# Kernel tuning notes

Hardware: AMD Instinct MI355X
Metric: run time of the kernel (lower is better)

Reference implementation:

```python
import jax, jax.numpy as jnp
import numpy as np

B, S, HID = 2, 4096, 1024
NH, HD = 16, 64
R = 2  # dilation_rate


def setup_inputs() -> dict:
    key = jax.random.key(0)
    ks = jax.random.split(key, 6)
    sc = 0.02
    return {
        "hidden_states": jax.random.normal(ks[0], (B, S, HID), jnp.float32),
        "Wq": jax.random.normal(ks[1], (HID, HID), jnp.float32) * sc,
        "Wk": jax.random.normal(ks[2], (HID, HID), jnp.float32) * sc,
        "Wv": jax.random.normal(ks[3], (HID, HID), jnp.float32) * sc,
        "Wo": jax.random.normal(ks[4], (HID, HID), jnp.float32) * sc,
        "bo": jnp.zeros((HID,), jnp.float32),
    }


def reference(hidden_states, Wq, Wk, Wv, Wo, bo):
    bsz, q_len, _ = hidden_states.shape
    # projections (torch Linear: y = x @ W.T)
    q = jnp.einsum('bsh,oh->bso', hidden_states, Wq).reshape(bsz, q_len, NH, HD).transpose(0, 2, 1, 3)
    k = jnp.einsum('bsh,oh->bso', hidden_states, Wk).reshape(bsz, q_len, NH, HD).transpose(0, 2, 1, 3)
    v = jnp.einsum('bsh,oh->bso', hidden_states, Wv).reshape(bsz, q_len, NH, HD).transpose(0, 2, 1, 3)
    # strided dilation gather (indices 0, R, 2R, ...)
    q = q[:, :, ::R, :]
    k = k[:, :, ::R, :]
    v = v[:, :, ::R, :]
    sd = q.shape[2]  # dilated length
    # SDPA with is_causal=True over the dilated subsequence
    scores = jnp.einsum('bhqd,bhkd->bhqk', q, k) / np.sqrt(HD).astype(np.float32)
    causal = jnp.tril(jnp.ones((sd, sd), bool))
    scores = jnp.where(causal, scores, jnp.finfo(scores.dtype).min)
    probs = jax.nn.softmax(scores, axis=-1)
    attn = jnp.einsum('bhqk,bhkd->bhqd', probs, v)  # [B, H, sd, HD]
    attn = attn.transpose(0, 2, 1, 3).reshape(bsz, sd, HID)
    # scatter back into zero-initialized full-length tensor
    full = jnp.zeros((bsz, q_len, HID), attn.dtype).at[:, ::R, :].set(attn)
    return jnp.einsum('bsh,oh->bso', full, Wo) + bo
```

## Files before the change

### kernel.cpp

```cpp
#include <hip/hip_runtime.h>
#include <cstdint>

typedef unsigned short u16;
typedef unsigned int u32;
typedef __attribute__((ext_vector_type(8))) short short8;
typedef __attribute__((ext_vector_type(4))) float f32x4;
typedef __attribute__((ext_vector_type(4))) unsigned short u16x4;
typedef __attribute__((ext_vector_type(4))) u32 u32x4;
typedef __attribute__((ext_vector_type(2))) u32 u32x2;

#define S_ 4096
#define SD 2048

__device__ __forceinline__ u16 f2bf(float f) {
  union { float f; u32 u; } v; v.f = f;
  u32 r = v.u + 0x7fffu + ((v.u >> 16) & 1u);
  return (u16)(r >> 16);
}
#if __has_builtin(__builtin_amdgcn_cvt_pk_bf16_f32)
__device__ __forceinline__ u32 pkbf(float a, float b) {
  auto r = __builtin_amdgcn_cvt_pk_bf16_f32(a, b);
  u32 o; __builtin_memcpy(&o, &r, 4); return o;
}
#else
__device__ __forceinline__ u32 pkbf(float a, float b) {
  union { float f; u32 u; } ua, ub; ua.f = a; ub.f = b;
  return __builtin_amdgcn_perm(ub.u + 0x8000u, ua.u + 0x8000u, 0x07060302u);
}
#endif
__device__ __forceinline__ f32x4 mfma16(short8 a, short8 b, f32x4 c) {
  return __builtin_amdgcn_mfma_f32_16x16x32_bf16(a, b, c, 0, 0, 0);
}
__device__ __forceinline__ void async16(const void* g, void* l) {
  __builtin_amdgcn_global_load_lds((__attribute__((address_space(1))) void*)g,
                                   (__attribute__((address_space(3))) void*)l,
                                   16, 0, 0);
}

__global__ __launch_bounds__(256) void cast_all(const float* __restrict__ hs,
                                                const float* __restrict__ Wq,
                                                const float* __restrict__ Wk,
                                                const float* __restrict__ Wv,
                                                const float* __restrict__ Wo,
                                                u16* __restrict__ dstW,
                                                u16* __restrict__ dstX) {
  int bid = blockIdx.x;
  if (bid < 4096) {
    int gid = bid * 256 + threadIdx.x;
    int wsel = gid >> 18;
    int off  = (gid & 262143) * 4;
    const float* src = (wsel == 0) ? Wq : (wsel == 1) ? Wk : (wsel == 2) ? Wv : Wo;
    float scl = (wsel == 0) ? 0.18033688f : 1.0f;
    f32x4 v = *(const f32x4*)(src + off);
    u16x4 o; o.x = f2bf(v.x * scl); o.y = f2bf(v.y * scl);
    o.z = f2bf(v.z * scl); o.w = f2bf(v.w * scl);
    *(u16x4*)(dstW + (size_t)wsel * 1048576 + off) = o;
  } else {
    int gid = (bid - 4096) * 256 + threadIdx.x;
    int e = gid * 4;
    int m = e >> 10, col = e & 1023;
    int b = m >> 11, sm = m & 2047;
    const float* src = hs + ((size_t)(b * S_ + 2 * sm) << 10) + col;
    f32x4 v = *(const f32x4*)src;
    u16x4 o; o.x = f2bf(v.x); o.y = f2bf(v.y); o.z = f2bf(v.z); o.w = f2bf(v.w);
    *(u16x4*)(dstX + ((size_t)m << 10) + col) = o;
  }
}

__device__ __forceinline__ void gemm_body128(const u16* __restrict__ A,
                                             const u16* __restrict__ B,
                                             u16* __restrict__ C, int N,
                                             int bm, int bn, char* lA, char* lB) {
  const int tid = threadIdx.x, lane = tid & 63, w = tid >> 6;
  const int quad = lane >> 4, l15 = lane & 15;
  const int wm = (w & 1) * 64, wn = (w >> 1) * 64;
  f32x4 acc[4][4] = {};

  auto stage = [&](int buf, int k0) {
#pragma unroll
    for (int i = 0; i < 2; i++) {
      int p = i * 256 + tid;
      int row = p >> 2, cp = p & 3;
      int c = cp ^ ((row ^ (row >> 2)) & 3);
      async16(A + (size_t)(bm + row) * 1024 + k0 + c * 8,
              lA + buf * 8192 + i * 4096 + w * 1024);
      async16(B + (size_t)(bn + row) * 1024 + k0 + c * 8,
              lB + buf * 8192 + i * 4096 + w * 1024);
    }
  };

  stage(0, 0);
#pragma unroll 1
  for (int kt = 0; kt < 32; kt++) {
    __syncthreads();
    if (kt + 1 < 32) stage((kt + 1) & 1, (kt + 1) * 32);
    const char* A_ = lA + (kt & 1) * 8192;
    const char* B_ = lB + (kt & 1) * 8192;
    short8 af[4], bf[4];
#pragma unroll
    for (int mi = 0; mi < 4; mi++) {
      int row = wm + mi * 16 + l15;
      af[mi] = *(const short8*)(A_ + (row * 4 + (quad ^ ((row ^ (row >> 2)) & 3))) * 16);
    }
#pragma unroll
    for (int ni = 0; ni < 4; ni++) {
      int row = wn + ni * 16 + l15;
      bf[ni] = *(const short8*)(B_ + (row * 4 + (quad ^ ((row ^ (row >> 2)) & 3))) * 16);
    }
#pragma unroll
    for (int mi = 0; mi < 4; mi++)
#pragma unroll
      for (int ni = 0; ni < 4; ni++)
        acc[mi][ni] = mfma16(af[mi], bf[ni], acc[mi][ni]);
  }
#pragma unroll
  for (int mi = 0; mi < 4; mi++)
#pragma unroll
    for (int ni = 0; ni < 4; ni++) {
      int m0 = bm + wm + mi * 16 + quad * 4;
      int n = bn + wn + ni * 16 + l15;
#pragma unroll
      for (int r = 0; r < 4; r++)
        C[(size_t)(m0 + r) * N + n] = f2bf(acc[mi][ni][r]);
    }
}

__global__ __launch_bounds__(256) void qkv_gemm(const u16* __restrict__ X,
                                                const u16* __restrict__ Wbf,
                                                u16* __restrict__ QK,
                                                u16* __restrict__ Vt) {
  __shared__ __align__(16) char lA[16384];
  __shared__ __align__(16) char lB[16384];
  int bid = blockIdx.x;
  if (bid < 512) {
    gemm_body128(X, Wbf, QK, 2048, (bid >> 4) * 128, (bid & 15) * 128, lA, lB);
  } else {
    int b2 = bid - 512;
    gemm_body128(Wbf + 2 * 1048576, X, Vt, 4096, (b2 >> 5) * 128, (b2 & 31) * 128, lA, lB);
  }
}

__global__ __launch_bounds__(256) void oproj(const u16* __restrict__ A,
                                             const u16* __restrict__ B,
                                             const float* __restrict__ bo,
                                             float* __restrict__ out) {
  __shared__ __align__(16) char lA[8192];
  __shared__ __align__(16) char lB[8192];
  const int tid = threadIdx.x, lane = tid & 63, w = tid >> 6;
  const int quad = lane >> 4, l15 = lane & 15;
  const int bm = blockIdx.y * 64, bn = blockIdx.x * 64;
  const int wm = (w & 1) * 32, wn = (w >> 1) * 32;
  f32x4 acc[2][2] = {};

  auto stage = [&](int buf, int k0) {
    int row = tid >> 2, cp = tid & 3;
    int c = cp ^ ((row ^ (row >> 2)) & 3);
    async16(A + (size_t)(bm + row) * 1024 + k0 + c * 8, lA + buf * 4096 + w * 1024);
    async16(B + (size_t)(bn + row) * 1024 + k0 + c * 8, lB + buf * 4096 + w * 1024);
  };

  stage(0, 0);
#pragma unroll 1
  for (int kt = 0; kt < 32; kt++) {
    __syncthreads();
    if (kt + 1 < 32) stage((kt + 1) & 1, (kt + 1) * 32);
    const char* A_ = lA + (kt & 1) * 4096;
    const char* B_ = lB + (kt & 1) * 4096;
    short8 af[2], bf[2];
#pragma unroll
    for (int mi = 0; mi < 2; mi++) {
      int row = wm + mi * 16 + l15;
      af[mi] = *(const short8*)(A_ + (row * 4 + (quad ^ ((row ^ (row >> 2)) & 3))) * 16);
    }
#pragma unroll
    for (int ni = 0; ni < 2; ni++) {
      int row = wn + ni * 16 + l15;
      bf[ni] = *(const short8*)(B_ + (row * 4 + (quad ^ ((row ^ (row >> 2)) & 3))) * 16);
    }
#pragma unroll
    for (int mi = 0; mi < 2; mi++)
#pragma unroll
      for (int ni = 0; ni < 2; ni++)
        acc[mi][ni] = mfma16(af[mi], bf[ni], acc[mi][ni]);
  }
#pragma unroll
  for (int mi = 0; mi < 2; mi++)
#pragma unroll
    for (int ni = 0; ni < 2; ni++) {
      int n = bn + wn + ni * 16 + l15;
      float bias = bo[n];
#pragma unroll
      for (int r = 0; r < 4; r++) {
        int m = bm + wm + mi * 16 + quad * 4 + r;
        int bb = m >> 11, sm = m & 2047;
        size_t grow = ((size_t)(bb * S_ + 2 * sm)) << 10;
        out[grow + n] = acc[mi][ni][r] + bias;
        out[grow + 1024 + n] = bias;
      }
    }
}

__global__ __launch_bounds__(256) void attn6(const u16* __restrict__ QK,
                                             const u16* __restrict__ Vt,
                                             u16* __restrict__ O) {
  __shared__ __align__(16) char lK[2][8192];
  __shared__ __align__(16) char lV[2][8192];
  const int tid = threadIdx.x, lane = tid & 63, w = tid >> 6;
  const int quad = lane >> 4, l15 = lane & 15;
  const int h = blockIdx.x, b = blockIdx.y;
  const int qt = 31 - (int)blockIdx.z;
  const int qb = qt * 64 + w * 16;

  const u16* qp = QK + (size_t)(b * SD + qb + l15) * 2048 + h * 64 + quad * 8;
  short8 qf0 = *(const short8*)qp;
  short8 qf1 = *(const short8*)(qp + 32);

  auto stageK = [&](int buf, int kb) {
#pragma unroll
    for (int i = 0; i < 2; i++) {
      int p = (w * 2 + i) * 64 + lane;
      int row = p >> 3, c = (p & 7) ^ (row & 7);
      async16(QK + (size_t)(b * SD + kb + row) * 2048 + 1024 + h * 64 + c * 8,
              lK[buf] + (w * 2 + i) * 1024);
    }
  };

  const int vd = tid >> 2, vg = tid & 3;
  const u16* vgbase = Vt + (size_t)(h * 64 + vd) * 4096 + b * SD;
  const int vs = vd & 7;
  const int cb0 = (vg & 1) * 2;
  const int cb1 = cb0 + 4;
  const int inn = (vg >> 1) * 8;
  const int aw0 = vd * 128 + ((cb0     ^ vs) * 16) + inn;
  const int aw1 = vd * 128 + (((cb0+1) ^ vs) * 16) + inn;
  const int aw2 = vd * 128 + ((cb1     ^ vs) * 16) + inn;
  const int aw3 = vd * 128 + (((cb1+1) ^ vs) * 16) + inn;

  u32x4 nv0, nv1;
  auto loadV = [&](int kb) {
    nv0 = *(const u32x4*)(vgbase + kb + vg * 8);
    nv1 = *(const u32x4*)(vgbase + kb + 32 + vg * 8);
  };
  auto writeV = [&](int buf) {
    char* Vn = lV[buf];
    *(u32x2*)(Vn + aw0) = u32x2{nv0.x, nv0.y};
    *(u32x2*)(Vn + aw1) = u32x2{nv0.z, nv0.w};
    *(u32x2*)(Vn + aw2) = u32x2{nv1.x, nv1.y};
    *(u32x2*)(Vn + aw3) = u32x2{nv1.z, nv1.w};
  };

  f32x4 oacc[4] = {};
  float l4[4] = {0.f, 0.f, 0.f, 0.f};

  stageK(0, 0);
  loadV(0);
  writeV(0);

#pragma unroll 1
  for (int kt = 0; kt <= qt; kt++) {
    __syncthreads();
    if (kt + 1 <= qt) {
      stageK((kt + 1) & 1, (kt + 1) * 64);
      loadV((kt + 1) * 64);
    }
    const char* K_ = lK[kt & 1];
    const char* V_ = lV[kt & 1];

    f32x4 s[4];
#pragma unroll
    for (int m = 0; m < 4; m++) {
      int key = m * 16 + l15;
      short8 kf0 = *(const short8*)(K_ + (key * 8 + (quad ^ (key & 7))) * 16);
      short8 kf1 = *(const short8*)(K_ + (key * 8 + ((4 + quad) ^ (key & 7))) * 16);
      f32x4 a = {};
      a = mfma16(kf0, qf0, a);
      a = mfma16(kf1, qf1, a);
      s[m] = a;
    }
    if (kt == qt) {
      int qrel = w * 16 + l15;
#pragma unroll
      for (int m = 0; m < 4; m++)
#pragma unroll
        for (int r = 0; r < 4; r++)
          if (m * 16 + quad * 4 + r > qrel) s[m][r] = -1e30f;
    }
    float pr[4][4];
#pragma unroll
    for (int m = 0; m < 4; m++) {
#pragma unroll
      for (int r = 0; r < 4; r++) pr[m][r] = exp2f(s[m][r]);
      l4[m] += (pr[m][0] + pr[m][1]) + (pr[m][2] + pr[m][3]);
    }
    u32 pw[8];
#pragma unroll
    for (int m = 0; m < 4; m++) {
      pw[m * 2]     = pkbf(pr[m][0], pr[m][1]);
      pw[m * 2 + 1] = pkbf(pr[m][2], pr[m][3]);
    }
    short8 pf0, pf1;
    __builtin_memcpy(&pf0, &pw[0], 16);
    __builtin_memcpy(&pf1, &pw[4], 16);

#pragma unroll
    for (int m = 0; m < 4; m++) {
      int dr = m * 16 + l15;
      short8 vf0 = *(const short8*)(V_ + (dr * 128 + ((quad     ^ (dr & 7)) * 16)));
      short8 vf1 = *(const short8*)(V_ + (dr * 128 + (((4+quad) ^ (dr & 7)) * 16)));
      oacc[m] = mfma16(vf0, pf0, oacc[m]);
      oacc[m] = mfma16(vf1, pf1, oacc[m]);
    }
    if (kt + 1 <= qt) writeV((kt + 1) & 1);
  }

  float l = (l4[0] + l4[1]) + (l4[2] + l4[3]);
  l += __shfl_xor(l, 16, 64);
  l += __shfl_xor(l, 32, 64);
  float inv = 1.0f / l;
  u16* op = O + (size_t)(b * SD + qb + l15) * 1024 + h * 64;
#pragma unroll
  for (int m = 0; m < 4; m++) {
    u16x4 ov;
#pragma unroll
    for (int r = 0; r < 4; r++) ov[r] = f2bf(oacc[m][r] * inv);
    *(u16x4*)(op + m * 16 + quad * 4) = ov;
  }
}

extern "C" void kernel_launch(void* const* d_in, const int* in_sizes, int n_in,
                              void* d_out, int out_size, void* d_ws, size_t ws_size,
                              hipStream_t stream) {
  (void)in_sizes; (void)n_in; (void)out_size; (void)ws_size;
  const float* hs = (const float*)d_in[0];
  const float* Wq = (const float*)d_in[1];
  const float* Wk = (const float*)d_in[2];
  const float* Wv = (const float*)d_in[3];
  const float* Wo = (const float*)d_in[4];
  const float* bo = (const float*)d_in[5];
  float* out = (float*)d_out;
  char* ws = (char*)d_ws;

  u16* Xbf = (u16*)ws;
  u16* Wbf = (u16*)(ws + (8u << 20));
  u16* QKb = (u16*)(ws + (16u << 20));
  u16* Vtb = (u16*)(ws + (32u << 20));
  u16* Ob  = (u16*)(ws + (40u << 20));

  cast_all<<<8192, 256, 0, stream>>>(hs, Wq, Wk, Wv, Wo, Wbf, Xbf);
  qkv_gemm<<<768, 256, 0, stream>>>(Xbf, Wbf, QKb, Vtb);
  attn6<<<dim3(16, 2, 32), 256, 0, stream>>>(QKb, Vtb, Ob);
  oproj<<<dim3(16, 64), 256, 0, stream>>>(Ob, Wbf + 3 * 1048576, bo, out);
}
```

Before: 190.6 us.

## Halve attention block to two waves each handling two query subtiles

The attention kernel now runs with 128 threads per block, and each wave computes two 16-row query subtiles. This lets every K and V fragment read from LDS feed twice as many MFMAs, cutting LDS traffic per FLOP. The V tile in LDS gains a padded row stride of 144 bytes to reduce bank conflicts, and exp2 now uses the hardware builtin when available. The trade-off is higher register pressure from doubled accumulators and fewer waves per block to hide latency.

```diff
diff --git a/kernel.cpp b/kernel.cpp
--- a/kernel.cpp
+++ b/kernel.cpp
@@ -27,6 +27,11 @@
   union { float f; u32 u; } ua, ub; ua.f = a; ub.f = b;
   return __builtin_amdgcn_perm(ub.u + 0x8000u, ua.u + 0x8000u, 0x07060302u);
 }
+#endif
+#if __has_builtin(__builtin_amdgcn_exp2f)
+__device__ __forceinline__ float fexp2(float x) { return __builtin_amdgcn_exp2f(x); }
+#else
+__device__ __forceinline__ float fexp2(float x) { return exp2f(x); }
 #endif
 __device__ __forceinline__ f32x4 mfma16(short8 a, short8 b, f32x4 c) {
   return __builtin_amdgcn_mfma_f32_16x16x32_bf16(a, b, c, 0, 0, 0);
@@ -200,57 +205,60 @@
     }
 }
 
-__global__ __launch_bounds__(256) void attn6(const u16* __restrict__ QK,
+#define VSTR 144
+__global__ __launch_bounds__(128) void attn7(const u16* __restrict__ QK,
                                              const u16* __restrict__ Vt,
                                              u16* __restrict__ O) {
   __shared__ __align__(16) char lK[2][8192];
-  __shared__ __align__(16) char lV[2][8192];
+  __shared__ __align__(16) char lV[2][64 * VSTR];
   const int tid = threadIdx.x, lane = tid & 63, w = tid >> 6;
   const int quad = lane >> 4, l15 = lane & 15;
   const int h = blockIdx.x, b = blockIdx.y;
   const int qt = 31 - (int)blockIdx.z;
-  const int qb = qt * 64 + w * 16;
-
-  const u16* qp = QK + (size_t)(b * SD + qb + l15) * 2048 + h * 64 + quad * 8;
-  short8 qf0 = *(const short8*)qp;
-  short8 qf1 = *(const short8*)(qp + 32);
+  const int qb = qt * 64;
+
+  short8 qf0[2], qf1[2];
+#pragma unroll
+  for (int s = 0; s < 2; s++) {
+    const u16* qp = QK + (size_t)(b * SD + qb + s * 32 + w * 16 + l15) * 2048 + h * 64 + quad * 8;
+    qf0[s] = *(const short8*)qp;
+    qf1[s] = *(const short8*)(qp + 32);
+  }
 
   auto stageK = [&](int buf, int kb) {
 #pragma unroll
-    for (int i = 0; i < 2; i++) {
-      int p = (w * 2 + i) * 64 + lane;
+    for (int i = 0; i < 4; i++) {
+      int p = i * 128 + tid;
       int row = p >> 3, c = (p & 7) ^ (row & 7);
       async16(QK + (size_t)(b * SD + kb + row) * 2048 + 1024 + h * 64 + c * 8,
-              lK[buf] + (w * 2 + i) * 1024);
-    }
-  };
-
-  const int vd = tid >> 2, vg = tid & 3;
+              lK[buf] + i * 2048 + w * 1024);
+    }
+  };
+
+  const int vd = tid >> 1, half = tid & 1;
+  const int vs = vd & 7;
   const u16* vgbase = Vt + (size_t)(h * 64 + vd) * 4096 + b * SD;
-  const int vs = vd & 7;
-  const int cb0 = (vg & 1) * 2;
-  const int cb1 = cb0 + 4;
-  const int inn = (vg >> 1) * 8;
-  const int aw0 = vd * 128 + ((cb0     ^ vs) * 16) + inn;
-  const int aw1 = vd * 128 + (((cb0+1) ^ vs) * 16) + inn;
-  const int aw2 = vd * 128 + ((cb1     ^ vs) * 16) + inn;
-  const int aw3 = vd * 128 + (((cb1+1) ^ vs) * 16) + inn;
-
-  u32x4 nv0, nv1;
+  u32x4 q0, q1, q2, q3;
   auto loadV = [&](int kb) {
-    nv0 = *(const u32x4*)(vgbase + kb + vg * 8);
-    nv1 = *(const u32x4*)(vgbase + kb + 32 + vg * 8);
+    q0 = *(const u32x4*)(vgbase + kb + half * 16);
+    q1 = *(const u32x4*)(vgbase + kb + half * 16 + 8);
+    q2 = *(const u32x4*)(vgbase + kb + 32 + half * 16);
+    q3 = *(const u32x4*)(vgbase + kb + 32 + half * 16 + 8);
   };
   auto writeV = [&](int buf) {
-    char* Vn = lV[buf];
-    *(u32x2*)(Vn + aw0) = u32x2{nv0.x, nv0.y};
-    *(u32x2*)(Vn + aw1) = u32x2{nv0.z, nv0.w};
-    *(u32x2*)(Vn + aw2) = u32x2{nv1.x, nv1.y};
-    *(u32x2*)(Vn + aw3) = u32x2{nv1.z, nv1.w};
-  };
-
-  f32x4 oacc[4] = {};
-  float l4[4] = {0.f, 0.f, 0.f, 0.f};
+    char* Vn = lV[buf] + vd * VSTR + half * 8;
+    *(u32x2*)(Vn + ((0 ^ vs) * 16)) = u32x2{q0.x, q0.y};
+    *(u32x2*)(Vn + ((1 ^ vs) * 16)) = u32x2{q0.z, q0.w};
+    *(u32x2*)(Vn + ((2 ^ vs) * 16)) = u32x2{q1.x, q1.y};
+    *(u32x2*)(Vn + ((3 ^ vs) * 16)) = u32x2{q1.z, q1.w};
+    *(u32x2*)(Vn + ((4 ^ vs) * 16)) = u32x2{q2.x, q2.y};
+    *(u32x2*)(Vn + ((5 ^ vs) * 16)) = u32x2{q2.z, q2.w};
+    *(u32x2*)(Vn + ((6 ^ vs) * 16)) = u32x2{q3.x, q3.y};
+    *(u32x2*)(Vn + ((7 ^ vs) * 16)) = u32x2{q3.z, q3.w};
+  };
+
+  f32x4 oacc[2][4] = {};
+  float l4[2][4] = {};
 
   stageK(0, 0);
   loadV(0);
@@ -266,64 +274,79 @@
     const char* K_ = lK[kt & 1];
     const char* V_ = lV[kt & 1];
 
-    f32x4 s[4];
+    f32x4 s[2][4];
 #pragma unroll
     for (int m = 0; m < 4; m++) {
       int key = m * 16 + l15;
       short8 kf0 = *(const short8*)(K_ + (key * 8 + (quad ^ (key & 7))) * 16);
       short8 kf1 = *(const short8*)(K_ + (key * 8 + ((4 + quad) ^ (key & 7))) * 16);
-      f32x4 a = {};
-      a = mfma16(kf0, qf0, a);
-      a = mfma16(kf1, qf1, a);
-      s[m] = a;
+#pragma unroll
+      for (int st = 0; st < 2; st++) {
+        f32x4 a = {};
+        a = mfma16(kf0, qf0[st], a);
+        a = mfma16(kf1, qf1[st], a);
+        s[st][m] = a;
+      }
     }
     if (kt == qt) {
-      int qrel = w * 16 + l15;
-#pragma unroll
-      for (int m = 0; m < 4; m++)
-#pragma unroll
-        for (int r = 0; r < 4; r++)
-          if (m * 16 + quad * 4 + r > qrel) s[m][r] = -1e30f;
-    }
-    float pr[4][4];
-#pragma unroll
-    for (int m = 0; m < 4; m++) {
-#pragma unroll
-      for (int r = 0; r < 4; r++) pr[m][r] = exp2f(s[m][r]);
-      l4[m] += (pr[m][0] + pr[m][1]) + (pr[m][2] + pr[m][3]);
-    }
-    u32 pw[8];
-#pragma unroll
-    for (int m = 0; m < 4; m++) {
-      pw[m * 2]     = pkbf(pr[m][0], pr[m][1]);
-      pw[m * 2 + 1] = pkbf(pr[m][2], pr[m][3]);
-    }
-    short8 pf0, pf1;
-    __builtin_memcpy(&pf0, &pw[0], 16);
-    __builtin_memcpy(&pf1, &pw[4], 16);
+#pragma unroll
+      for (int st = 0; st < 2; st++) {
+        int qrel = st * 32 + w * 16 + l15;
+#pragma unroll
+        for (int m = 0; m < 4; m++)
+#pragma unroll
+          for (int r = 0; r < 4; r++)
+            if (m * 16 + quad * 4 + r > qrel) s[st][m][r] = -1e30f;
+      }
+    }
+    short8 pf0[2], pf1[2];
+#pragma unroll
+    for (int st = 0; st < 2; st++) {
+      float pr[4][4];
+#pragma unroll
+      for (int m = 0; m < 4; m++) {
+#pragma unroll
+        for (int r = 0; r < 4; r++) pr[m][r] = fexp2(s[st][m][r]);
+        l4[st][m] += (pr[m][0] + pr[m][1]) + (pr[m][2] + pr[m][3]);
+      }
+      u32 pw[8];
+#pragma unroll
+      for (int m = 0; m < 4; m++) {
+        pw[m * 2]     = pkbf(pr[m][0], pr[m][1]);
+        pw[m * 2 + 1] = pkbf(pr[m][2], pr[m][3]);
+      }
+      __builtin_memcpy(&pf0[st], &pw[0], 16);
+      __builtin_memcpy(&pf1[st], &pw[4], 16);
+    }
 
 #pragma unroll
     for (int m = 0; m < 4; m++) {
       int dr = m * 16 + l15;
-      short8 vf0 = *(const short8*)(V_ + (dr * 128 + ((quad     ^ (dr & 7)) * 16)));
-      short8 vf1 = *(const short8*)(V_ + (dr * 128 + (((4+quad) ^ (dr & 7)) * 16)));
-      oacc[m] = mfma16(vf0, pf0, oacc[m]);
-      oacc[m] = mfma16(vf1, pf1, oacc[m]);
+      short8 vf0 = *(const short8*)(V_ + dr * VSTR + ((quad       ^ (dr & 7)) * 16));
+      short8 vf1 = *(const short8*)(V_ + dr * VSTR + (((4 + quad) ^ (dr & 7)) * 16));
+#pragma unroll
+      for (int st = 0; st < 2; st++) {
+        oacc[st][m] = mfma16(vf0, pf0[st], oacc[st][m]);
+        oacc[st][m] = mfma16(vf1, pf1[st], oacc[st][m]);
+      }
     }
     if (kt + 1 <= qt) writeV((kt + 1) & 1);
   }
 
-  float l = (l4[0] + l4[1]) + (l4[2] + l4[3]);
-  l += __shfl_xor(l, 16, 64);
-  l += __shfl_xor(l, 32, 64);
-  float inv = 1.0f / l;
-  u16* op = O + (size_t)(b * SD + qb + l15) * 1024 + h * 64;
-#pragma unroll
-  for (int m = 0; m < 4; m++) {
-    u16x4 ov;
-#pragma unroll
-    for (int r = 0; r < 4; r++) ov[r] = f2bf(oacc[m][r] * inv);
-    *(u16x4*)(op + m * 16 + quad * 4) = ov;
+#pragma unroll
+  for (int st = 0; st < 2; st++) {
+    float l = (l4[st][0] + l4[st][1]) + (l4[st][2] + l4[st][3]);
+    l += __shfl_xor(l, 16, 64);
+    l += __shfl_xor(l, 32, 64);
+    float inv = 1.0f / l;
+    u16* op = O + (size_t)(b * SD + qb + st * 32 + w * 16 + l15) * 1024 + h * 64;
+#pragma unroll
+    for (int m = 0; m < 4; m++) {
+      u16x4 ov;
+#pragma unroll
+      for (int r = 0; r < 4; r++) ov[r] = f2bf(oacc[st][m][r] * inv);
+      *(u16x4*)(op + m * 16 + quad * 4) = ov;
+    }
   }
 }
 
@@ -348,6 +371,6 @@
 
   cast_all<<<8192, 256, 0, stream>>>(hs, Wq, Wk, Wv, Wo, Wbf, Xbf);
   qkv_gemm<<<768, 256, 0, stream>>>(Xbf, Wbf, QKb, Vtb);
-  attn6<<<dim3(16, 2, 32), 256, 0, stream>>>(QKb, Vtb, Ob);
+  attn7<<<dim3(16, 2, 32), 128, 0, stream>>>(QKb, Vtb, Ob);
   oproj<<<dim3(16, 64), 256, 0, stream>>>(Ob, Wbf + 3 * 1048576, bo, out);
 }
```

New measurement: 199.5 us. +4.7%, slower.
